# Optimization experiments

Measured on AMD Instinct MI355X. Metric: run time of the kernel, lower is better.

Reference implementation:

```python
import jax, jax.numpy as jnp
import numpy as np

RATIO = 1.0
IGNORE_INDEX = 255
N, C, H, W = 8, 19, 512, 1024


def setup_inputs() -> dict:
    key = jax.random.key(0)
    k1, k2 = jax.random.split(key)
    inputs = jax.random.normal(k1, (N, C, H, W), dtype=jnp.float32)
    targets = jax.random.randint(k2, (N, H, W), 0, C, dtype=jnp.int32)
    return {"inputs": inputs, "targets": targets}


def reference(inputs, targets):
    n, c, h, w = inputs.shape
    logp = jax.nn.log_softmax(inputs, axis=1)  # [N,C,H,W]

    # Per-sample class histogram over labels in [0, C-1]
    # (torch.histc with bins=C, min=0, max=C-1 excludes out-of-range values like 255).
    in_range = (targets >= 0) & (targets < c)               # [N,H,W]
    t_safe = jnp.where(in_range, targets, 0)
    flat_idx = (t_safe + jnp.arange(n, dtype=t_safe.dtype)[:, None, None] * c).ravel()
    hist = jnp.zeros(n * c, dtype=jnp.float32).at[flat_idx].add(
        in_range.ravel().astype(jnp.float32)).reshape(n, c)
    hist = jnp.where(hist == 0, 1.0, hist)                  # hist[hist==0] = 1
    weight = (hist.sum(axis=1, keepdims=True) / hist) ** RATIO  # [N,C], sum taken AFTER zero-fill

    # NLL with per-sample class weights folded into log-probs, ignore_index masked.
    valid = targets != IGNORE_INDEX                          # [N,H,W]
    t_clamped = jnp.where(valid, targets, 0)
    logp_t = jnp.take_along_axis(logp, t_clamped[:, None], axis=1)[:, 0]        # [N,H,W]
    w_t = jnp.take_along_axis(weight, t_clamped.reshape(n, -1), axis=1).reshape(n, h, w)
    per_pix = -logp_t * w_t
    valid_f = valid.astype(per_pix.dtype)
    # reduction='mean' in F.nll_loss (no class weight arg): divide by #valid pixels
    loss = jnp.sum(per_pix * valid_f) / jnp.maximum(jnp.sum(valid_f), 1.0)
    return loss
```

## Files before the change

### kernel.cpp

```cpp
#include <hip/hip_runtime.h>
#include <math.h>

#define N_  8
#define C_  19
#define H_  512
#define W_  1024
#define HW_ (H_ * W_)
#define NPIX (N_ * HW_)
#define IGNORE_IDX 255

#define WS_HIST_OFF   0
#define WS_VALID_OFF  608
#define WS_LOSS_OFF   616
#define WS_ZERO_BYTES 1024

__global__ __launch_bounds__(256) void hist_kernel(
    const int* __restrict__ tgt, int* __restrict__ hist, int* __restrict__ valid_cnt) {
  __shared__ int lhist[N_ * C_];
  __shared__ int lvalid;
  const int tid = threadIdx.x;
  for (int i = tid; i < N_ * C_; i += blockDim.x) lhist[i] = 0;
  if (tid == 0) lvalid = 0;
  __syncthreads();

  int lv = 0;
  const int total4 = NPIX / 4;
  for (int i = blockIdx.x * blockDim.x + tid; i < total4;
       i += gridDim.x * blockDim.x) {
    const int4 t4 = reinterpret_cast<const int4*>(tgt)[i];
    const int n = (i * 4) / HW_;
    const int tv[4] = {t4.x, t4.y, t4.z, t4.w};
#pragma unroll
    for (int j = 0; j < 4; ++j) {
      if (tv[j] != IGNORE_IDX) ++lv;
      if (tv[j] >= 0 && tv[j] < C_) atomicAdd(&lhist[n * C_ + tv[j]], 1);
    }
  }
  atomicAdd(&lvalid, lv);
  __syncthreads();

  for (int i = tid; i < N_ * C_; i += blockDim.x)
    if (lhist[i] != 0) atomicAdd(&hist[i], lhist[i]);
  if (tid == 0) atomicAdd(valid_cnt, lvalid);
}

__global__ __launch_bounds__(256) void loss_kernel(
    const float* __restrict__ x, const int* __restrict__ tgt,
    const int* __restrict__ hist, double* __restrict__ loss_sum) {
  __shared__ float lw[C_];
  const int tid = threadIdx.x;
  const int n = blockIdx.x >> 9;

  if (tid < C_) {
    int s = 0;
#pragma unroll
    for (int c = 0; c < C_; ++c) s += max(hist[n * C_ + c], 1);
    lw[tid] = (float)s / (float)max(hist[n * C_ + tid], 1);
  }
  __syncthreads();

  const int hw4 = ((blockIdx.x & 511) << 8) + tid;
  const size_t hw = (size_t)hw4 * 4;

  const float4* xb =
      reinterpret_cast<const float4*>(x + ((size_t)n * C_) * HW_ + hw);
  const size_t cstride = HW_ / 4;

  float4 v[C_];
  float4 m = make_float4(-INFINITY, -INFINITY, -INFINITY, -INFINITY);
#pragma unroll
  for (int c = 0; c < C_; ++c) {
    v[c] = xb[(size_t)c * cstride];
    m.x = fmaxf(m.x, v[c].x);
    m.y = fmaxf(m.y, v[c].y);
    m.z = fmaxf(m.z, v[c].z);
    m.w = fmaxf(m.w, v[c].w);
  }

  const int4 t4 = reinterpret_cast<const int4*>(tgt)[(size_t)n * cstride + hw4];
  const int t[4] = {t4.x, t4.y, t4.z, t4.w};
  bool valid[4];
  int tc[4];
#pragma unroll
  for (int j = 0; j < 4; ++j) {
    valid[j] = (t[j] != IGNORE_IDX);
    tc[j] = valid[j] ? min(max(t[j], 0), C_ - 1) : 0;
  }

  float4 s = make_float4(0.f, 0.f, 0.f, 0.f);
  float xt0 = 0.f, xt1 = 0.f, xt2 = 0.f, xt3 = 0.f;
#pragma unroll
  for (int c = 0; c < C_; ++c) {
    s.x += expf(v[c].x - m.x);
    s.y += expf(v[c].y - m.y);
    s.z += expf(v[c].z - m.z);
    s.w += expf(v[c].w - m.w);
    xt0 = (c == tc[0]) ? v[c].x : xt0;
    xt1 = (c == tc[1]) ? v[c].y : xt1;
    xt2 = (c == tc[2]) ? v[c].z : xt2;
    xt3 = (c == tc[3]) ? v[c].w : xt3;
  }

  const float lse0 = m.x + logf(s.x);
  const float lse1 = m.y + logf(s.y);
  const float lse2 = m.z + logf(s.z);
  const float lse3 = m.w + logf(s.w);

  double acc = 0.0;
  acc += valid[0] ? (double)((lse0 - xt0) * lw[tc[0]]) : 0.0;
  acc += valid[1] ? (double)((lse1 - xt1) * lw[tc[1]]) : 0.0;
  acc += valid[2] ? (double)((lse2 - xt2) * lw[tc[2]]) : 0.0;
  acc += valid[3] ? (double)((lse3 - xt3) * lw[tc[3]]) : 0.0;

#pragma unroll
  for (int off = 32; off > 0; off >>= 1) acc += __shfl_down(acc, off, 64);
  __shared__ double wsum[4];
  const int wid = tid >> 6, lane = tid & 63;
  if (lane == 0) wsum[wid] = acc;
  __syncthreads();
  if (tid == 0) atomicAdd(loss_sum, wsum[0] + wsum[1] + wsum[2] + wsum[3]);
}

__global__ void finalize_kernel(const double* __restrict__ loss_sum,
                                const int* __restrict__ valid_cnt,
                                float* __restrict__ out) {
  if (threadIdx.x == 0 && blockIdx.x == 0) {
    const double denom = fmax((double)valid_cnt[0], 1.0);
    out[0] = (float)(loss_sum[0] / denom);
  }
}

extern "C" void kernel_launch(void* const* d_in, const int* in_sizes, int n_in,
                              void* d_out, int out_size, void* d_ws, size_t ws_size,
                              hipStream_t stream) {
  const float* inputs = (const float*)d_in[0];
  const int* targets = (const int*)d_in[1];
  float* out = (float*)d_out;

  int* hist = (int*)((char*)d_ws + WS_HIST_OFF);
  int* valid_cnt = (int*)((char*)d_ws + WS_VALID_OFF);
  double* loss_sum = (double*)((char*)d_ws + WS_LOSS_OFF);

  hipMemsetAsync(d_ws, 0, WS_ZERO_BYTES, stream);

  hist_kernel<<<1024, 256, 0, stream>>>(targets, hist, valid_cnt);

  loss_kernel<<<4096, 256, 0, stream>>>(inputs, targets, hist, loss_sum);

  finalize_kernel<<<1, 1, 0, stream>>>(loss_sum, valid_cnt, out);
}
```

Baseline: 502.1 us.

## Use ballot-based histogram and online softmax with two float4 pixels per thread

The histogram kernel drops per-element LDS atomics. Each block now covers one sample segment and counts classes with wavefront ballots and popcounts, then issues one LDS atomic per wave per class. The loss kernel switches to an online (streaming) log-sum-exp with fast __expf/__logf intrinsics and handles 8 pixels per thread, so it no longer keeps all 19 channel vectors live. This lowers register pressure, frees the loads to stream, and cuts expensive transcendental calls, at the cost of slightly lower precision from the fast intrinsics and an extra exp per channel for rescaling.

```diff
diff --git a/kernel.cpp b/kernel.cpp
--- a/kernel.cpp
+++ b/kernel.cpp
@@ -16,32 +16,45 @@
 
 __global__ __launch_bounds__(256) void hist_kernel(
     const int* __restrict__ tgt, int* __restrict__ hist, int* __restrict__ valid_cnt) {
-  __shared__ int lhist[N_ * C_];
+  __shared__ int lh[C_];
   __shared__ int lvalid;
   const int tid = threadIdx.x;
-  for (int i = tid; i < N_ * C_; i += blockDim.x) lhist[i] = 0;
+  if (tid < C_) lh[tid] = 0;
   if (tid == 0) lvalid = 0;
   __syncthreads();
 
-  int lv = 0;
-  const int total4 = NPIX / 4;
-  for (int i = blockIdx.x * blockDim.x + tid; i < total4;
-       i += gridDim.x * blockDim.x) {
-    const int4 t4 = reinterpret_cast<const int4*>(tgt)[i];
-    const int n = (i * 4) / HW_;
+  const int n = blockIdx.x >> 6;
+  const int seg = blockIdx.x & 63;
+  const int4* tp = reinterpret_cast<const int4*>(tgt) +
+                   (size_t)n * (HW_ / 4) + (size_t)seg * 2048;
+
+  int cnt[C_];
+#pragma unroll
+  for (int c = 0; c < C_; ++c) cnt[c] = 0;
+  int vcnt = 0;
+
+#pragma unroll
+  for (int it = 0; it < 8; ++it) {
+    const int4 t4 = tp[it * 256 + tid];
     const int tv[4] = {t4.x, t4.y, t4.z, t4.w};
 #pragma unroll
     for (int j = 0; j < 4; ++j) {
-      if (tv[j] != IGNORE_IDX) ++lv;
-      if (tv[j] >= 0 && tv[j] < C_) atomicAdd(&lhist[n * C_ + tv[j]], 1);
+      vcnt += (int)__popcll(__ballot(tv[j] != IGNORE_IDX));
+#pragma unroll
+      for (int c = 0; c < C_; ++c)
+        cnt[c] += (int)__popcll(__ballot(tv[j] == c));
     }
   }
-  atomicAdd(&lvalid, lv);
+
+  if ((tid & 63) == 0) {
+#pragma unroll
+    for (int c = 0; c < C_; ++c)
+      if (cnt[c]) atomicAdd(&lh[c], cnt[c]);
+    atomicAdd(&lvalid, vcnt);
+  }
   __syncthreads();
-
-  for (int i = tid; i < N_ * C_; i += blockDim.x)
-    if (lhist[i] != 0) atomicAdd(&hist[i], lhist[i]);
-  if (tid == 0) atomicAdd(valid_cnt, lvalid);
+  if (tid < C_ && lh[tid]) atomicAdd(&hist[n * C_ + tid], lh[tid]);
+  if (tid == 0 && lvalid) atomicAdd(valid_cnt, lvalid);
 }
 
 __global__ __launch_bounds__(256) void loss_kernel(
@@ -49,7 +62,7 @@
     const int* __restrict__ hist, double* __restrict__ loss_sum) {
   __shared__ float lw[C_];
   const int tid = threadIdx.x;
-  const int n = blockIdx.x >> 9;
+  const int n = blockIdx.x >> 8;
 
   if (tid < C_) {
     int s = 0;
@@ -59,58 +72,52 @@
   }
   __syncthreads();
 
-  const int hw4 = ((blockIdx.x & 511) << 8) + tid;
-  const size_t hw = (size_t)hw4 * 4;
+  const int blk = blockIdx.x & 255;
+  const int q0 = blk * 512 + tid;
+  const int q1 = q0 + 256;
+  const float* xb = x + (size_t)n * C_ * HW_;
 
-  const float4* xb =
-      reinterpret_cast<const float4*>(x + ((size_t)n * C_) * HW_ + hw);
-  const size_t cstride = HW_ / 4;
+  const int4* tq = reinterpret_cast<const int4*>(tgt + (size_t)n * HW_);
+  const int4 ta = tq[q0];
+  const int4 tb = tq[q1];
+  const int t[8] = {ta.x, ta.y, ta.z, ta.w, tb.x, tb.y, tb.z, tb.w};
+  bool val[8];
+  int tc[8];
+#pragma unroll
+  for (int j = 0; j < 8; ++j) {
+    val[j] = (t[j] != IGNORE_IDX);
+    tc[j] = val[j] ? min(max(t[j], 0), C_ - 1) : 0;
+  }
 
-  float4 v[C_];
-  float4 m = make_float4(-INFINITY, -INFINITY, -INFINITY, -INFINITY);
+  float m[8], s[8], xt[8];
+#pragma unroll
+  for (int j = 0; j < 8; ++j) {
+    m[j] = -INFINITY;
+    s[j] = 0.f;
+    xt[j] = 0.f;
+  }
+
 #pragma unroll
   for (int c = 0; c < C_; ++c) {
-    v[c] = xb[(size_t)c * cstride];
-    m.x = fmaxf(m.x, v[c].x);
-    m.y = fmaxf(m.y, v[c].y);
-    m.z = fmaxf(m.z, v[c].z);
-    m.w = fmaxf(m.w, v[c].w);
+    const float4* xc = reinterpret_cast<const float4*>(xb + (size_t)c * HW_);
+    const float4 va = xc[q0];
+    const float4 vb = xc[q1];
+    const float v[8] = {va.x, va.y, va.z, va.w, vb.x, vb.y, vb.z, vb.w};
+#pragma unroll
+    for (int j = 0; j < 8; ++j) {
+      const float nm = fmaxf(m[j], v[j]);
+      s[j] = s[j] * __expf(m[j] - nm) + __expf(v[j] - nm);
+      m[j] = nm;
+      xt[j] = (c == tc[j]) ? v[j] : xt[j];
+    }
   }
 
-  const int4 t4 = reinterpret_cast<const int4*>(tgt)[(size_t)n * cstride + hw4];
-  const int t[4] = {t4.x, t4.y, t4.z, t4.w};
-  bool valid[4];
-  int tc[4];
+  double acc = 0.0;
 #pragma unroll
-  for (int j = 0; j < 4; ++j) {
-    valid[j] = (t[j] != IGNORE_IDX);
-    tc[j] = valid[j] ? min(max(t[j], 0), C_ - 1) : 0;
+  for (int j = 0; j < 8; ++j) {
+    const float lse = m[j] + __logf(s[j]);
+    acc += val[j] ? (double)((lse - xt[j]) * lw[tc[j]]) : 0.0;
   }
-
-  float4 s = make_float4(0.f, 0.f, 0.f, 0.f);
-  float xt0 = 0.f, xt1 = 0.f, xt2 = 0.f, xt3 = 0.f;
-#pragma unroll
-  for (int c = 0; c < C_; ++c) {
-    s.x += expf(v[c].x - m.x);
-    s.y += expf(v[c].y - m.y);
-    s.z += expf(v[c].z - m.z);
-    s.w += expf(v[c].w - m.w);
-    xt0 = (c == tc[0]) ? v[c].x : xt0;
-    xt1 = (c == tc[1]) ? v[c].y : xt1;
-    xt2 = (c == tc[2]) ? v[c].z : xt2;
-    xt3 = (c == tc[3]) ? v[c].w : xt3;
-  }
-
-  const float lse0 = m.x + logf(s.x);
-  const float lse1 = m.y + logf(s.y);
-  const float lse2 = m.z + logf(s.z);
-  const float lse3 = m.w + logf(s.w);
-
-  double acc = 0.0;
-  acc += valid[0] ? (double)((lse0 - xt0) * lw[tc[0]]) : 0.0;
-  acc += valid[1] ? (double)((lse1 - xt1) * lw[tc[1]]) : 0.0;
-  acc += valid[2] ? (double)((lse2 - xt2) * lw[tc[2]]) : 0.0;
-  acc += valid[3] ? (double)((lse3 - xt3) * lw[tc[3]]) : 0.0;
 
 #pragma unroll
   for (int off = 32; off > 0; off >>= 1) acc += __shfl_down(acc, off, 64);
@@ -143,9 +150,9 @@
 
   hipMemsetAsync(d_ws, 0, WS_ZERO_BYTES, stream);
 
-  hist_kernel<<<1024, 256, 0, stream>>>(targets, hist, valid_cnt);
+  hist_kernel<<<512, 256, 0, stream>>>(targets, hist, valid_cnt);
 
-  loss_kernel<<<4096, 256, 0, stream>>>(inputs, targets, hist, loss_sum);
+  loss_kernel<<<2048, 256, 0, stream>>>(inputs, targets, hist, loss_sum);
 
   finalize_kernel<<<1, 1, 0, stream>>>(loss_sum, valid_cnt, out);
 }
```

After: 469.1 us. 1.07x faster.
